# Optimization experiments

Hardware: AMD Instinct MI355X
Metric: run time of the kernel (lower is better)

The kernel has to match this reference:

```python
import jax, jax.numpy as jnp
import numpy as np
import math


def _extend(chunk):
    # chunk: [b, C, w, 1, dh] -> stacked (prev, cur, next) chunks: [b, C, w, 1, dh, 3]
    prev = jnp.pad(chunk[:, :-1], ((0, 0), (1, 0), (0, 0), (0, 0), (0, 0)))
    nxt = jnp.pad(chunk[:, 1:], ((0, 0), (0, 1), (0, 0), (0, 0), (0, 0)))
    return jnp.stack((prev, chunk, nxt), axis=-1)


def local_xl_attention(q, kv, Wq, Wkv, Wc, w):
    b, L, dm = q.shape
    dh = Wkv.shape[1] // 2          # d_head (w_kv projects to 2*d_head)
    nh = dm // dh                   # n_head
    C = L // w                      # number of chunks

    qp = (q @ Wq).reshape(b, L, nh, dh) / math.sqrt(dh)   # [b,L,nh,dh]
    kvp = kv @ Wkv                                         # [b,L,2*dh]
    k = kvp[..., :dh][:, :, None, :]                       # [b,L,1,dh] single KV head
    v = kvp[..., dh:][:, :, None, :]

    # sliding_chunks_matmul_qk (faithful to original einsum, incl. sum over z)
    cq = qp.reshape(b, C, w, nh, dh)
    ck_e = _extend(k.reshape(b, C, w, 1, dh))              # [b,C,w,1,dh,3]
    attn = jnp.einsum('bcxhd,bzyode->bcxhey', cq, ck_e)    # [b,C,w,nh,3,w]
    attn = attn.reshape(b, L, nh, 3 * w)

    probs = jax.nn.softmax(attn, axis=-1)

    # sliding_chunks_matmul_pv (faithful, incl. sum over z)
    cp = probs.reshape(b, C, w, nh, 3, w)
    cv_e = _extend(v.reshape(b, C, w, 1, dh))              # [b,C,w,1,dh,3]
    ctx = jnp.einsum('bcwhpd,bzdoep->bcwhe', cp, cv_e)     # [b,C,w,nh,dh]
    out = ctx.reshape(b, L, dm) @ Wc
    return out


def setup_inputs() -> dict:
    key = jax.random.key(0)
    ks = jax.random.split(key, 5)
    B, L, DM, NH = 1, 4096, 1024, 16
    DH = DM // NH
    scale = 0.02
    return {
        'q': jax.random.normal(ks[0], (B, L, DM), dtype=jnp.float32),
        'kv': jax.random.normal(ks[1], (B, L, DM), dtype=jnp.float32),
        'Wq': jax.random.normal(ks[2], (DM, DM), dtype=jnp.float32) * scale,
        'Wkv': jax.random.normal(ks[3], (DM, 2 * DH), dtype=jnp.float32) * scale,
        'Wc': jax.random.normal(ks[4], (DM, DM), dtype=jnp.float32) * scale,
        'w': 512,
    }


def reference(q, kv, Wq, Wkv, Wc, w):
    return local_xl_attention(q, kv, Wq, Wkv, Wc, w)
```

## Files before the change

kernel.cpp:

```cpp
#include <hip/hip_runtime.h>
#include <hip/hip_bf16.h>
#include <cstdint>
#include <cstddef>

#define L_ 4096
#define DM_ 1024
#define NH_ 16
#define DH_ 64
#define W_ 512
#define C_ 8
#define W3_ 1536
#define NROWS_ 65536

typedef __attribute__((ext_vector_type(8))) short short8;
typedef __attribute__((ext_vector_type(4))) float f32x4;

__device__ __forceinline__ void async16(const void* g, void* l) {
    __builtin_amdgcn_global_load_lds(
        (const __attribute__((address_space(1))) unsigned int*)g,
        (__attribute__((address_space(3))) unsigned int*)l, 16, 0, 0);
}

#if __has_builtin(__builtin_amdgcn_exp2f)
#define FEXP2(x) __builtin_amdgcn_exp2f(x)
#else
#define FEXP2(x) exp2f(x)
#endif

__device__ __forceinline__ int nanhit(unsigned u) {
    return (((u & 0x7F80u) == 0x7F80u) | (((u >> 16) & 0x7F80u) == 0x7F80u));
}
__global__ __launch_bounds__(256) void detect_kernel(const uint4* __restrict__ q,
                                                     int* __restrict__ flag) {
    __shared__ int s;
    if (threadIdx.x == 0) s = 0;
    __syncthreads();
    int hit = 0;
#pragma unroll
    for (int r = 0; r < 8; ++r) {
        uint4 v = q[threadIdx.x + 256 * r];
        hit |= nanhit(v.x) | nanhit(v.y) | nanhit(v.z) | nanhit(v.w);
    }
    if (__any(hit)) { if ((threadIdx.x & 63) == 0) atomicOr(&s, 1); }
    __syncthreads();
    if (threadIdx.x == 0) flag[0] = s;
}

__device__ __forceinline__ float ldf(const void* X, size_t i, int f32) {
    return f32 ? ((const float*)X)[i] : __bfloat162float(((const __hip_bfloat16*)X)[i]);
}

__global__ __launch_bounds__(256) void megaprep(const void* __restrict__ q,
                                                const void* __restrict__ kv,
                                                const void* __restrict__ Wq,
                                                const void* __restrict__ Wkv,
                                                const void* __restrict__ Wc,
                                                __hip_bfloat16* __restrict__ qbuf,
                                                __hip_bfloat16* __restrict__ WqT,
                                                __hip_bfloat16* __restrict__ WkvT,
                                                __hip_bfloat16* __restrict__ WcT,
                                                __hip_bfloat16* __restrict__ kvred,
                                                const int* __restrict__ flag) {
    __shared__ float t[64][65];
    const int b = blockIdx.x;
    const int f32 = flag[0];
    const int tid = threadIdx.x;

    if (b < 4096) {
        int i = (b * 256 + tid) * 4;
        if (f32) {
            float4 v = *(const float4*)((const float*)q + i);
            __hip_bfloat162 tmp[2] = {__float22bfloat162_rn({v.x, v.y}),
                                      __float22bfloat162_rn({v.z, v.w})};
            *(short4*)((short*)qbuf + i) = *(const short4*)tmp;
        } else {
            *(short4*)((short*)qbuf + i) = *(const short4*)((const short*)q + i);
        }
    } else if (b < 4640) {
        const void* W;
        __hip_bfloat16* WT;
        int K = 1024, N, n0, k0;
        if (b < 4352) {
            int bx = b - 4096; W = Wq; WT = WqT; N = 1024;
            n0 = (bx & 15) * 64; k0 = (bx >> 4) * 64;
        } else if (b < 4608) {
            int bx = b - 4352; W = Wc; WT = WcT; N = 1024;
            n0 = (bx & 15) * 64; k0 = (bx >> 4) * 64;
        } else {
            int bx = b - 4608; W = Wkv; WT = WkvT; N = 128;
            n0 = (bx & 1) * 64; k0 = (bx >> 1) * 64;
        }
        const int tx = tid & 63;
        const int ty = tid >> 6;
#pragma unroll
        for (int r = 0; r < 16; ++r) {
            int k = ty + r * 4;
            t[k][tx] = ldf(W, (size_t)(k0 + k) * N + n0 + tx, f32);
        }
        __syncthreads();
#pragma unroll
        for (int r = 0; r < 16; ++r) {
            int n = ty + r * 4;
            WT[(size_t)(n0 + n) * K + k0 + tx] = __float2bfloat16(t[tx][n]);
        }
    } else {
        int y2 = b - 4640;
        int c = tid * 4;
        float a0 = 0.f, a1 = 0.f, a2 = 0.f, a3 = 0.f;
        if (y2 < 512) {
#pragma unroll
            for (int z = 0; z < C_; ++z) {
                size_t base = (size_t)(z * W_ + y2) * 1024 + c;
                a0 += ldf(kv, base + 0, f32);
                a1 += ldf(kv, base + 1, f32);
                a2 += ldf(kv, base + 2, f32);
                a3 += ldf(kv, base + 3, f32);
            }
        } else {
            int row = (y2 < 1024) ? (y2 - 512) : (3584 + y2 - 1024);
            size_t base = (size_t)row * 1024 + c;
            a0 = ldf(kv, base + 0, f32);
            a1 = ldf(kv, base + 1, f32);
            a2 = ldf(kv, base + 2, f32);
            a3 = ldf(kv, base + 3, f32);
        }
        __hip_bfloat162 tmp[2] = {__float22bfloat162_rn({a0, a1}),
                                  __float22bfloat162_rn({a2, a3})};
        *(short4*)((short*)kvred + (size_t)y2 * 1024 + c) = *(const short4*)tmp;
    }
}

struct GemmP {
    const __hip_bfloat16* A;
    const __hip_bfloat16* BT;
    void* C;
    int M, N, K;
    float alpha;
    int cMode;
    int ntiles;
    int swz;
    int nblocks;
};

__global__ __launch_bounds__(256) void gemm_bt_mfma(GemmP p0, GemmP p1,
                                                    const int* __restrict__ flag) {
    __shared__ __hip_bfloat16 Asl[2][128 * 32];
    __shared__ __hip_bfloat16 Bsl[2][64 * 32];

    GemmP p;
    int bid;
    if ((int)blockIdx.x < p0.nblocks) { p = p0; bid = blockIdx.x; }
    else { p = p1; bid = (int)blockIdx.x - p0.nblocks; }

    int mt, nt;
    if (!p.swz) { mt = bid / p.ntiles; nt = bid % p.ntiles; }
    else {
        int g = bid / (8 * p.ntiles);
        int rem = bid % (8 * p.ntiles);
        mt = g * 8 + (rem & 7);
        nt = rem >> 3;
    }
    const int m0 = mt * 128;
    const int n0 = nt * 64;
    const int K = p.K;
    const int N = p.N;

    const int tid = threadIdx.x;
    const int lane = tid & 63;
    const int wv = tid >> 6;
    const int wm = wv >> 1;
    const int wn = wv & 1;
    const int col = lane & 15;
    const int quad = lane >> 4;

    const int srow = lane >> 2;
    const int scol = (lane & 3) * 8;
    const __hip_bfloat16* Ag = p.A + (size_t)m0 * K;
    const __hip_bfloat16* Bg = p.BT + (size_t)n0 * K;

    f32x4 acc[4][2] = {};

    for (int k0 = 0; k0 < K; k0 += 64) {
#pragma unroll
        for (int h = 0; h < 2; ++h) {
            int arow = wv * 32 + h * 16 + srow;
#pragma unroll
            for (int kc = 0; kc < 2; ++kc)
                async16(Ag + (size_t)arow * K + k0 + kc * 32 + scol,
                        &Asl[kc][arow * 32 + scol]);
        }
        {
            int brow = wv * 16 + srow;
#pragma unroll
            for (int kc = 0; kc < 2; ++kc)
                async16(Bg + (size_t)brow * K + k0 + kc * 32 + scol,
                        &Bsl[kc][brow * 32 + scol]);
        }
        __syncthreads();

#pragma unroll
        for (int kc = 0; kc < 2; ++kc) {
            short8 af[4], bfr[2];
#pragma unroll
            for (int i = 0; i < 4; ++i)
                af[i] = *(const short8*)(&Asl[kc][(wm * 64 + i * 16 + col) * 32 + quad * 8]);
#pragma unroll
            for (int j = 0; j < 2; ++j)
                bfr[j] = *(const short8*)(&Bsl[kc][(wn * 32 + j * 16 + col) * 32 + quad * 8]);
#pragma unroll
            for (int am = 0; am < 4; ++am)
#pragma unroll
                for (int bn = 0; bn < 2; ++bn)
                    acc[am][bn] = __builtin_amdgcn_mfma_f32_16x16x32_bf16(af[am], bfr[bn], acc[am][bn], 0, 0, 0);
        }
        __syncthreads();
    }

    int cF = (p.cMode == 1) ? 1 : ((p.cMode == 2) ? 0 : flag[0]);
#pragma unroll
    for (int am = 0; am < 4; ++am)
#pragma unroll
        for (int bn = 0; bn < 2; ++bn)
#pragma unroll
            for (int r = 0; r < 4; ++r) {
                size_t ci = (size_t)(m0 + wm * 64 + am * 16 + quad * 4 + r) * N
                            + n0 + wn * 32 + bn * 16 + col;
                float v = acc[am][bn][r] * p.alpha;
                if (cF) ((float*)p.C)[ci] = v;
                else ((__hip_bfloat16*)p.C)[ci] = __float2bfloat16(v);
            }
}

__global__ __launch_bounds__(256) void sums_kernel(const float* __restrict__ kvp_red,
                                                   char* __restrict__ Kb,
                                                   char* __restrict__ Vt) {
    int t = blockIdx.x * 256 + threadIdx.x;
    int d = t & 63;
    int y = t >> 6;

    float kc = kvp_red[(size_t)y * 128 + d];
    float kf = kvp_red[(size_t)(512 + y) * 128 + d];
    float kl = kvp_red[(size_t)(1024 + y) * 128 + d];
    float vc = kvp_red[(size_t)y * 128 + 64 + d];
    float vf = kvp_red[(size_t)(512 + y) * 128 + 64 + d];
    float vl = kvp_red[(size_t)(1024 + y) * 128 + 64 + d];

    float kvals[3] = {kc - kl, kc, kc - kf};
    float vvals[3] = {vc - vl, vc, vc - vf};
#pragma unroll
    for (int e = 0; e < 3; ++e) {
        int key = e * W_ + y;
        int g = key >> 6;
        int r = key & 63;
        int kbyte = g * 8192 + r * 128 + ((((d >> 3) ^ (r & 7)) << 4)) + ((d & 7) << 1);
        *(__hip_bfloat16*)(Kb + kbyte) = __float2bfloat16(kvals[e]);
        int p = ((r & 15) << 2) | (r >> 4);
        int vbyte = g * 8192 + d * 128 + ((((p >> 3) ^ (d & 7)) << 4)) + ((p & 7) << 1);
        *(__hip_bfloat16*)(Vt + vbyte) = __float2bfloat16(vvals[e]);
    }
}

#define PSTRIDE 72
__global__ __launch_bounds__(256, 3) void attn_kernel(const __hip_bfloat16* __restrict__ qb,
                                                      const __hip_bfloat16* __restrict__ Kb,
                                                      const __hip_bfloat16* __restrict__ Vt,
                                                      __hip_bfloat16* __restrict__ ctx) {
    __shared__ __align__(16) __hip_bfloat16 Kbuf[2][4096];
    __shared__ __align__(16) __hip_bfloat16 Vbuf[2][4096];
    __shared__ __align__(16) __hip_bfloat16 psm[4][16 * PSTRIDE];

    const int tid = threadIdx.x;
    const int lane = tid & 63;
    const int wv = tid >> 6;
    const int m0 = blockIdx.x * 64 + wv * 16;
    const int col = lane & 15;
    const int quad = lane >> 4;
    __hip_bfloat16* pw = psm[wv];

    const char* Kg = (const char*)Kb;
    const char* Vg = (const char*)Vt;
    const int so = tid * 16;

    const int off0 = ((quad ^ (col & 7)) << 4);
    const int off1 = (((quad + 4) ^ (col & 7)) << 4);

    short8 qf0, qf1;
    {
        const __hip_bfloat16* qp = qb + (size_t)(m0 + col) * 64 + quad * 8;
        qf0 = *(const short8*)(qp);
        qf1 = *(const short8*)(qp + 32);
    }

    f32x4 O[4] = {};
    float lrow[4] = {};

    async16(Kg + so, (char*)Kbuf[0] + so);
    async16(Kg + 4096 + so, (char*)Kbuf[0] + 4096 + so);
    async16(Vg + so, (char*)Vbuf[0] + so);
    async16(Vg + 4096 + so, (char*)Vbuf[0] + 4096 + so);
    __syncthreads();

    for (int t = 0; t < 24; ++t) {
        const int cur = t & 1;
        if (t < 23) {
            const char* ks = Kg + (size_t)(t + 1) * 8192;
            const char* vs = Vg + (size_t)(t + 1) * 8192;
            char* kd = (char*)Kbuf[cur ^ 1];
            char* vd = (char*)Vbuf[cur ^ 1];
            async16(ks + so, kd + so);
            async16(ks + 4096 + so, kd + 4096 + so);
            async16(vs + so, vd + so);
            async16(vs + 4096 + so, vd + 4096 + so);
        }
        const char* Kc = (const char*)Kbuf[cur];
        const char* Vc = (const char*)Vbuf[cur];

        short8 kb0[4], kb1[4];
#pragma unroll
        for (int f = 0; f < 4; ++f) {
            const int rb = (f * 16 + col) * 128;
            kb0[f] = *(const short8*)(Kc + rb + off0);
            kb1[f] = *(const short8*)(Kc + rb + off1);
        }

        f32x4 S[4];
        __builtin_amdgcn_s_setprio(1);
#pragma unroll
        for (int f = 0; f < 4; ++f) {
            f32x4 s = {};
            s = __builtin_amdgcn_mfma_f32_16x16x32_bf16(qf0, kb0[f], s, 0, 0, 0);
            s = __builtin_amdgcn_mfma_f32_16x16x32_bf16(qf1, kb1[f], s, 0, 0, 0);
            S[f] = s;
        }
        __builtin_amdgcn_s_setprio(0);
#pragma unroll
        for (int f = 0; f < 4; ++f)
#pragma unroll
            for (int r = 0; r < 4; ++r) S[f][r] = FEXP2(S[f][r]);
#pragma unroll
        for (int r = 0; r < 4; ++r)
            lrow[r] += (S[0][r] + S[1][r]) + (S[2][r] + S[3][r]);
#pragma unroll
        for (int r = 0; r < 4; ++r) {
            __hip_bfloat162 p01 = __float22bfloat162_rn({S[0][r], S[1][r]});
            __hip_bfloat162 p23 = __float22bfloat162_rn({S[2][r], S[3][r]});
            short4 t4;
            *(__hip_bfloat162*)(&t4.x) = p01;
            *(__hip_bfloat162*)(&t4.z) = p23;
            *(short4*)(pw + (quad * 4 + r) * PSTRIDE + col * 4) = t4;
        }

        short8 vb0[4], vb1[4];
#pragma unroll
        for (int f = 0; f < 4; ++f) {
            const int rb = (f * 16 + col) * 128;
            vb0[f] = *(const short8*)(Vc + rb + off0);
            vb1[f] = *(const short8*)(Vc + rb + off1);
        }

        short8 a0 = *(const short8*)(pw + col * PSTRIDE + quad * 8);
        short8 a1 = *(const short8*)(pw + col * PSTRIDE + 32 + quad * 8);
        __builtin_amdgcn_s_setprio(1);
#pragma unroll
        for (int f = 0; f < 4; ++f) {
            O[f] = __builtin_amdgcn_mfma_f32_16x16x32_bf16(a0, vb0[f], O[f], 0, 0, 0);
            O[f] = __builtin_amdgcn_mfma_f32_16x16x32_bf16(a1, vb1[f], O[f], 0, 0, 0);
        }
        __builtin_amdgcn_s_setprio(0);

        __syncthreads();
    }

#pragma unroll
    for (int msk = 1; msk <= 8; msk <<= 1)
#pragma unroll
        for (int r = 0; r < 4; ++r) lrow[r] += __shfl_xor(lrow[r], msk, 64);

#pragma unroll
    for (int r = 0; r < 4; ++r) {
        float inv = 1.f / lrow[r];
#pragma unroll
        for (int f = 0; f < 4; ++f)
            ctx[(size_t)(m0 + quad * 4 + r) * 64 + f * 16 + col] =
                __float2bfloat16(O[f][r] * inv);
    }
}

extern "C" void kernel_launch(void* const* d_in, const int* in_sizes, int n_in,
                              void* d_out, int out_size, void* d_ws, size_t ws_size,
                              hipStream_t stream) {
    const void* q   = d_in[0];
    const void* kv  = d_in[1];
    const void* Wq  = d_in[2];
    const void* Wkv = d_in[3];
    const void* Wc  = d_in[4];

    char* ws = (char*)d_ws;
    size_t off = 0;
    int* flag = (int*)(ws + off); off += 1024;
    __hip_bfloat16* qbuf   = (__hip_bfloat16*)(ws + off); off += (size_t)L_ * DM_ * 2;
    __hip_bfloat16* WqT    = (__hip_bfloat16*)(ws + off); off += (size_t)DM_ * DM_ * 2;
    __hip_bfloat16* WkvT   = (__hip_bfloat16*)(ws + off); off += (size_t)128 * DM_ * 2;
    __hip_bfloat16* WcT    = (__hip_bfloat16*)(ws + off); off += (size_t)DM_ * DM_ * 2;
    __hip_bfloat16* qb     = (__hip_bfloat16*)(ws + off); off += (size_t)L_ * DM_ * 2;
    __hip_bfloat16* kvred  = (__hip_bfloat16*)(ws + off); off += (size_t)1536 * 1024 * 2;
    float*          kvpred = (float*)(ws + off);          off += (size_t)1536 * 128 * 4;
    __hip_bfloat16* Kb     = (__hip_bfloat16*)(ws + off); off += (size_t)W3_ * 64 * 2;
    __hip_bfloat16* Vt     = (__hip_bfloat16*)(ws + off); off += (size_t)64 * W3_ * 2;
    __hip_bfloat16* ctxb   = (__hip_bfloat16*)(ws + off);

    detect_kernel<<<1, 256, 0, stream>>>((const uint4*)q, flag);

    megaprep<<<6176, 256, 0, stream>>>(q, kv, Wq, Wkv, Wc,
                                       qbuf, WqT, WkvT, WcT, kvred, flag);

    {
        GemmP pq{qbuf, WqT, (void*)qb, L_, DM_, DM_,
                 0.125f * 1.44269504f, 2, 16, 1, 512};
        GemmP pk{kvred, WkvT, (void*)kvpred, 1536, 128, DM_,
                 1.0f, 1, 2, 0, 24};
        gemm_bt_mfma<<<536, 256, 0, stream>>>(pq, pk, flag);
    }
    sums_kernel<<<128, 256, 0, stream>>>(kvpred, (char*)Kb, (char*)Vt);
    attn_kernel<<<dim3(NROWS_ / 64), 256, 0, stream>>>(qb, Kb, Vt, ctxb);
    {
        GemmP pc{ctxb, WcT, d_out, L_, DM_, DM_, 1.0f, 0, 16, 1, 512};
        GemmP pnull{};
        pnull.nblocks = 0;
        gemm_bt_mfma<<<512, 256, 0, stream>>>(pc, pnull, flag);
    }
}
```

Before: 188.5 us.

## Fold dtype detection into prep, precombine KV rows, and fuse sums into GEMM epilogue

Drops the separate detect kernel: every megaprep block now re-reads the first part of q to work out the input dtype on its own, and block 0 writes the flag. The KV reduction now does the chunk-boundary subtractions (sum minus last, sum, sum minus first) before the projection GEMM, which works because the projection is linear. That lets the KV GEMM write swizzled K and transposed V directly through a new epilogue mode, and removes sums_kernel and the fp32 intermediate. The cost is two fewer launches and less intermediate traffic in exchange for redundant small q reads per block, a different bf16 rounding order, and megaprep reading kv with 8 loads per block for all 512 row blocks.

```diff
diff --git a/kernel.cpp b/kernel.cpp
--- a/kernel.cpp
+++ b/kernel.cpp
@@ -29,21 +29,6 @@
 
 __device__ __forceinline__ int nanhit(unsigned u) {
     return (((u & 0x7F80u) == 0x7F80u) | (((u >> 16) & 0x7F80u) == 0x7F80u));
-}
-__global__ __launch_bounds__(256) void detect_kernel(const uint4* __restrict__ q,
-                                                     int* __restrict__ flag) {
-    __shared__ int s;
-    if (threadIdx.x == 0) s = 0;
-    __syncthreads();
-    int hit = 0;
-#pragma unroll
-    for (int r = 0; r < 8; ++r) {
-        uint4 v = q[threadIdx.x + 256 * r];
-        hit |= nanhit(v.x) | nanhit(v.y) | nanhit(v.z) | nanhit(v.w);
-    }
-    if (__any(hit)) { if ((threadIdx.x & 63) == 0) atomicOr(&s, 1); }
-    __syncthreads();
-    if (threadIdx.x == 0) flag[0] = s;
 }
 
 __device__ __forceinline__ float ldf(const void* X, size_t i, int f32) {
@@ -59,12 +44,27 @@
                                                 __hip_bfloat16* __restrict__ WqT,
                                                 __hip_bfloat16* __restrict__ WkvT,
                                                 __hip_bfloat16* __restrict__ WcT,
-                                                __hip_bfloat16* __restrict__ kvred,
-                                                const int* __restrict__ flag) {
+                                                __hip_bfloat16* __restrict__ kvcomb,
+                                                int* __restrict__ flag) {
     __shared__ float t[64][65];
+    __shared__ int sflag;
     const int b = blockIdx.x;
-    const int f32 = flag[0];
     const int tid = threadIdx.x;
+
+    if (tid == 0) sflag = 0;
+    __syncthreads();
+    {
+        int hit = 0;
+#pragma unroll
+        for (int r = 0; r < 4; ++r) {
+            uint4 v = ((const uint4*)q)[tid + 256 * r];
+            hit |= nanhit(v.x) | nanhit(v.y) | nanhit(v.z) | nanhit(v.w);
+        }
+        if (__any(hit)) { if ((tid & 63) == 0) atomicOr(&sflag, 1); }
+    }
+    __syncthreads();
+    const int f32 = sflag;
+    if (b == 0 && tid == 0) flag[0] = f32;
 
     if (b < 4096) {
         int i = (b * 256 + tid) * 4;
@@ -104,29 +104,37 @@
             WT[(size_t)(n0 + n) * K + k0 + tx] = __float2bfloat16(t[tx][n]);
         }
     } else {
-        int y2 = b - 4640;
+        int y = b - 4640;
         int c = tid * 4;
-        float a0 = 0.f, a1 = 0.f, a2 = 0.f, a3 = 0.f;
-        if (y2 < 512) {
-#pragma unroll
-            for (int z = 0; z < C_; ++z) {
-                size_t base = (size_t)(z * W_ + y2) * 1024 + c;
-                a0 += ldf(kv, base + 0, f32);
-                a1 += ldf(kv, base + 1, f32);
-                a2 += ldf(kv, base + 2, f32);
-                a3 += ldf(kv, base + 3, f32);
+        float s0 = 0, s1 = 0, s2 = 0, s3 = 0;
+        float f0 = 0, f1 = 0, f2 = 0, f3 = 0;
+        float l0 = 0, l1 = 0, l2 = 0, l3 = 0;
+#pragma unroll
+        for (int z = 0; z < C_; ++z) {
+            size_t base = (size_t)(z * W_ + y) * 1024 + c;
+            float a0, a1, a2, a3;
+            if (f32) {
+                float4 v = *(const float4*)((const float*)kv + base);
+                a0 = v.x; a1 = v.y; a2 = v.z; a3 = v.w;
+            } else {
+                short4 v = *(const short4*)((const short*)kv + base);
+                a0 = __bfloat162float(*(__hip_bfloat16*)&v.x);
+                a1 = __bfloat162float(*(__hip_bfloat16*)&v.y);
+                a2 = __bfloat162float(*(__hip_bfloat16*)&v.z);
+                a3 = __bfloat162float(*(__hip_bfloat16*)&v.w);
             }
-        } else {
-            int row = (y2 < 1024) ? (y2 - 512) : (3584 + y2 - 1024);
-            size_t base = (size_t)row * 1024 + c;
-            a0 = ldf(kv, base + 0, f32);
-            a1 = ldf(kv, base + 1, f32);
-            a2 = ldf(kv, base + 2, f32);
-            a3 = ldf(kv, base + 3, f32);
-        }
-        __hip_bfloat162 tmp[2] = {__float22bfloat162_rn({a0, a1}),
-                                  __float22bfloat162_rn({a2, a3})};
-        *(short4*)((short*)kvred + (size_t)y2 * 1024 + c) = *(const short4*)tmp;
+            s0 += a0; s1 += a1; s2 += a2; s3 += a3;
+            if (z == 0) { f0 = a0; f1 = a1; f2 = a2; f3 = a3; }
+            if (z == C_ - 1) { l0 = a0; l1 = a1; l2 = a2; l3 = a3; }
+        }
+        auto store = [&](int row, float x0, float x1, float x2, float x3) {
+            __hip_bfloat162 tmp[2] = {__float22bfloat162_rn({x0, x1}),
+                                      __float22bfloat162_rn({x2, x3})};
+            *(short4*)((short*)kvcomb + (size_t)row * 1024 + c) = *(const short4*)tmp;
+        };
+        store(y,        s0 - l0, s1 - l1, s2 - l2, s3 - l3);
+        store(512 + y,  s0, s1, s2, s3);
+        store(1024 + y, s0 - f0, s1 - f1, s2 - f2, s3 - f3);
     }
 }
 
@@ -140,6 +148,7 @@
     int ntiles;
     int swz;
     int nblocks;
+    void* C2;
 };
 
 __global__ __launch_bounds__(256) void gemm_bt_mfma(GemmP p0, GemmP p1,
@@ -216,6 +225,32 @@
         __syncthreads();
     }
 
+    if (p.cMode == 3) {
+#pragma unroll
+        for (int am = 0; am < 4; ++am)
+#pragma unroll
+            for (int bn = 0; bn < 2; ++bn)
+#pragma unroll
+                for (int r = 0; r < 4; ++r) {
+                    int key = m0 + wm * 64 + am * 16 + quad * 4 + r;
+                    int c = n0 + wn * 32 + bn * 16 + col;
+                    float v = acc[am][bn][r];
+                    int g = key >> 6, kr = key & 63;
+                    if (c < 64) {
+                        int byt = g * 8192 + kr * 128 +
+                                  ((((c >> 3) ^ (kr & 7)) << 4)) + ((c & 7) << 1);
+                        *(__hip_bfloat16*)((char*)p.C + byt) = __float2bfloat16(v);
+                    } else {
+                        int d = c - 64;
+                        int pp = ((kr & 15) << 2) | (kr >> 4);
+                        int byt = g * 8192 + d * 128 +
+                                  ((((pp >> 3) ^ (d & 7)) << 4)) + ((pp & 7) << 1);
+                        *(__hip_bfloat16*)((char*)p.C2 + byt) = __float2bfloat16(v);
+                    }
+                }
+        return;
+    }
+
     int cF = (p.cMode == 1) ? 1 : ((p.cMode == 2) ? 0 : flag[0]);
 #pragma unroll
     for (int am = 0; am < 4; ++am)
@@ -229,35 +264,6 @@
                 if (cF) ((float*)p.C)[ci] = v;
                 else ((__hip_bfloat16*)p.C)[ci] = __float2bfloat16(v);
             }
-}
-
-__global__ __launch_bounds__(256) void sums_kernel(const float* __restrict__ kvp_red,
-                                                   char* __restrict__ Kb,
-                                                   char* __restrict__ Vt) {
-    int t = blockIdx.x * 256 + threadIdx.x;
-    int d = t & 63;
-    int y = t >> 6;
-
-    float kc = kvp_red[(size_t)y * 128 + d];
-    float kf = kvp_red[(size_t)(512 + y) * 128 + d];
-    float kl = kvp_red[(size_t)(1024 + y) * 128 + d];
-    float vc = kvp_red[(size_t)y * 128 + 64 + d];
-    float vf = kvp_red[(size_t)(512 + y) * 128 + 64 + d];
-    float vl = kvp_red[(size_t)(1024 + y) * 128 + 64 + d];
-
-    float kvals[3] = {kc - kl, kc, kc - kf};
-    float vvals[3] = {vc - vl, vc, vc - vf};
-#pragma unroll
-    for (int e = 0; e < 3; ++e) {
-        int key = e * W_ + y;
-        int g = key >> 6;
-        int r = key & 63;
-        int kbyte = g * 8192 + r * 128 + ((((d >> 3) ^ (r & 7)) << 4)) + ((d & 7) << 1);
-        *(__hip_bfloat16*)(Kb + kbyte) = __float2bfloat16(kvals[e]);
-        int p = ((r & 15) << 2) | (r >> 4);
-        int vbyte = g * 8192 + d * 128 + ((((p >> 3) ^ (d & 7)) << 4)) + ((p & 7) << 1);
-        *(__hip_bfloat16*)(Vt + vbyte) = __float2bfloat16(vvals[e]);
-    }
 }
 
 #define PSTRIDE 72
@@ -403,28 +409,24 @@
     __hip_bfloat16* WkvT   = (__hip_bfloat16*)(ws + off); off += (size_t)128 * DM_ * 2;
     __hip_bfloat16* WcT    = (__hip_bfloat16*)(ws + off); off += (size_t)DM_ * DM_ * 2;
     __hip_bfloat16* qb     = (__hip_bfloat16*)(ws + off); off += (size_t)L_ * DM_ * 2;
-    __hip_bfloat16* kvred  = (__hip_bfloat16*)(ws + off); off += (size_t)1536 * 1024 * 2;
-    float*          kvpred = (float*)(ws + off);          off += (size_t)1536 * 128 * 4;
+    __hip_bfloat16* kvcomb = (__hip_bfloat16*)(ws + off); off += (size_t)1536 * 1024 * 2;
     __hip_bfloat16* Kb     = (__hip_bfloat16*)(ws + off); off += (size_t)W3_ * 64 * 2;
     __hip_bfloat16* Vt     = (__hip_bfloat16*)(ws + off); off += (size_t)64 * W3_ * 2;
     __hip_bfloat16* ctxb   = (__hip_bfloat16*)(ws + off);
 
-    detect_kernel<<<1, 256, 0, stream>>>((const uint4*)q, flag);
-
-    megaprep<<<6176, 256, 0, stream>>>(q, kv, Wq, Wkv, Wc,
-                                       qbuf, WqT, WkvT, WcT, kvred, flag);
+    megaprep<<<5152, 256, 0, stream>>>(q, kv, Wq, Wkv, Wc,
+                                       qbuf, WqT, WkvT, WcT, kvcomb, flag);
 
     {
         GemmP pq{qbuf, WqT, (void*)qb, L_, DM_, DM_,
-                 0.125f * 1.44269504f, 2, 16, 1, 512};
-        GemmP pk{kvred, WkvT, (void*)kvpred, 1536, 128, DM_,
-                 1.0f, 1, 2, 0, 24};
+                 0.125f * 1.44269504f, 2, 16, 1, 512, nullptr};
+        GemmP pk{kvcomb, WkvT, (void*)Kb, 1536, 128, DM_,
+                 1.0f, 3, 2, 0, 24, (void*)Vt};
         gemm_bt_mfma<<<536, 256, 0, stream>>>(pq, pk, flag);
     }
-    sums_kernel<<<128, 256, 0, stream>>>(kvpred, (char*)Kb, (char*)Vt);
     attn_kernel<<<dim3(NROWS_ / 64), 256, 0, stream>>>(qb, Kb, Vt, ctxb);
     {
-        GemmP pc{ctxb, WcT, d_out, L_, DM_, DM_, 1.0f, 0, 16, 1, 512};
+        GemmP pc{ctxb, WcT, d_out, L_, DM_, DM_, 1.0f, 0, 16, 1, 512, nullptr};
         GemmP pnull{};
         pnull.nblocks = 0;
         gemm_bt_mfma<<<512, 256, 0, stream>>>(pc, pnull, flag);
```

After: 182.2 us. -3.3%, faster.
